# Optimization experiments

Hardware: AMD Instinct MI355X
Metric: run time of the kernel (lower is better)

## Reference

```python
import jax, jax.numpy as jnp
import numpy as np

DIM = 1024        # model dim
HEADS = 1         # num_heads (fc1 in_features==1 forces this)
HDIM = DIM // HEADS
INNER = 16        # dim_inner
B, L = 2, 4096
ROPE_BASE = 32.0


def _apply_rope(x, pos, base):
    # x: [b, l, h, d]; standard rotate-half RoPE
    d = x.shape[-1]
    inv_freq = base ** (-jnp.arange(0, d, 2, dtype=jnp.float32) / d)   # [d/2]
    ang = pos[:, None].astype(jnp.float32) * inv_freq                  # [l, d/2]
    emb = jnp.concatenate([ang, ang], axis=-1)                         # [l, d]
    cos = jnp.cos(emb)[None, :, None, :].astype(x.dtype)
    sin = jnp.sin(emb)[None, :, None, :].astype(x.dtype)
    x1, x2 = x[..., : d // 2], x[..., d // 2:]
    rot = jnp.concatenate([-x2, x1], axis=-1)
    return x * cos + rot * sin


def setup_inputs() -> dict:
    key = jax.random.key(0)
    ks = jax.random.split(key, 7)
    hidden_states = jax.random.normal(ks[0], (B, L, DIM), dtype=jnp.float32)
    Wq = jax.random.normal(ks[1], (DIM, DIM), dtype=jnp.float32) * 0.02
    Wk = jax.random.normal(ks[2], (DIM, DIM), dtype=jnp.float32) * 0.02
    fc1_w = jax.random.normal(ks[3], (INNER, 1), dtype=jnp.float32) * 0.1
    fc1_b = jax.random.normal(ks[4], (INNER,), dtype=jnp.float32) * 0.1
    fc2_w = jax.random.normal(ks[5], (DIM, INNER), dtype=jnp.float32) * 0.1
    fc2_b = jax.random.normal(ks[6], (DIM,), dtype=jnp.float32) * 0.1
    return {"hidden_states": hidden_states, "Wq": Wq, "Wk": Wk,
            "fc1_w": fc1_w, "fc1_b": fc1_b, "fc2_w": fc2_w, "fc2_b": fc2_b}


def reference(hidden_states, Wq, Wk, fc1_w, fc1_b, fc2_w, fc2_b):
    b, l, _ = hidden_states.shape
    # projections, cast to bf16 as in the torch module
    q = (hidden_states @ Wq.T).reshape(b, l, HEADS, HDIM).astype(jnp.bfloat16)
    k = (hidden_states @ Wk.T).reshape(b, l, HEADS, HDIM).astype(jnp.bfloat16)
    pos = jnp.arange(l)
    q = _apply_rope(q, pos, ROPE_BASE)
    k = _apply_rope(k, pos, ROPE_BASE)
    # causal exp(QK) with NO softmax normalization; accumulate in fp32
    scores = jnp.einsum('bqhd,bkhd->bhqk',
                        q.astype(jnp.float32), k.astype(jnp.float32)) / (HDIM ** 0.5)
    causal = jnp.tril(jnp.ones((l, l), dtype=bool))                    # [l, l]
    exp_qk = jnp.where(causal[None, None], jnp.exp(scores), 0.0)       # [b, h, l, l]
    o = jnp.swapaxes(exp_qk.sum(axis=-1), 1, 2)                        # [b, l, h]
    # small MLP: h(=1) -> INNER -> DIM
    o = jax.nn.relu(o @ fc1_w.T + fc1_b)
    return o @ fc2_w.T + fc2_b                                         # [b, l, DIM]
```

## Files before the change

kernel.cpp:

```cpp
#include <hip/hip_runtime.h>
#include <hip/hip_bf16.h>

typedef __bf16 bf16_t;
typedef __bf16 bf16x4 __attribute__((ext_vector_type(4)));
typedef __bf16 bf16x8 __attribute__((ext_vector_type(8)));
typedef float f32x4 __attribute__((ext_vector_type(4)));

#define B_   2
#define L_   4096
#define DIM_ 1024
#define M_   (B_ * L_)
#define MT_  (L_ / 128)
#define NTASK_ ((MT_ * (MT_ + 1)) / 2)

__device__ __forceinline__ void ld_g2l_16(const bf16_t* g, bf16_t* l) {
  __builtin_amdgcn_global_load_lds(
      (__attribute__((address_space(1))) void*)g,
      (__attribute__((address_space(3))) void*)l, 16, 0, 0);
}

__global__ void cvt_f32_bf16(const float* __restrict__ src,
                             bf16_t* __restrict__ dst, int n4) {
  int i = blockIdx.x * blockDim.x + threadIdx.x;
  if (i < n4) {
    float4 v = ((const float4*)src)[i];
    bf16x4 o = { (bf16_t)v.x, (bf16_t)v.y, (bf16_t)v.z, (bf16_t)v.w };
    ((bf16x4*)dst)[i] = o;
  }
}

__device__ __forceinline__ void mfma_bt_core(const bf16_t* __restrict__ A,
                                             const bf16_t* __restrict__ B,
                                             int K, bf16_t* As, bf16_t* Bs,
                                             f32x4 (&acc)[4][4]) {
  const int tid  = threadIdx.x;
  const int wave = tid >> 6, lane = tid & 63;
  const int quad = lane >> 4, l16 = lane & 15;
  const int wm = (wave >> 1) * 64, wn = (wave & 1) * 64;
  const int srow = lane >> 2;
  const int scol = (lane & 3) * 8;

  for (int kk = 0; kk < K; kk += 32) {
    __syncthreads();
#pragma unroll
    for (int c = 0; c < 2; ++c) {
      int seg = c * 4 + wave;
      int row = seg * 16 + srow;
      ld_g2l_16(A + (size_t)row * K + kk + scol, As + seg * 512);
      ld_g2l_16(B + (size_t)row * K + kk + scol, Bs + seg * 512);
    }
    __syncthreads();

    bf16x8 af[4], bfr[4];
#pragma unroll
    for (int i = 0; i < 4; ++i) {
      af[i]  = *(const bf16x8*)(As + (wm + i * 16 + l16) * 32 + quad * 8);
      bfr[i] = *(const bf16x8*)(Bs + (wn + i * 16 + l16) * 32 + quad * 8);
    }
#pragma unroll
    for (int i = 0; i < 4; ++i)
#pragma unroll
      for (int j = 0; j < 4; ++j)
        acc[i][j] = __builtin_amdgcn_mfma_f32_16x16x32_bf16(af[i], bfr[j],
                                                            acc[i][j], 0, 0, 0);
  }
}

__global__ __launch_bounds__(256)
void proj_gemm(const bf16_t* __restrict__ A, const bf16_t* __restrict__ Wqb,
               const bf16_t* __restrict__ Wkb, bf16_t* __restrict__ Cq,
               bf16_t* __restrict__ Ck) {
  const int K = DIM_, N = DIM_;
  const bf16_t* Bm = (blockIdx.z == 0) ? Wqb : Wkb;
  bf16_t* Cm = (blockIdx.z == 0) ? Cq : Ck;
  __shared__ __attribute__((aligned(16))) bf16_t As[128 * 32];
  __shared__ __attribute__((aligned(16))) bf16_t Bs[128 * 32];
  const int tid = threadIdx.x;
  const int wave = tid >> 6, lane = tid & 63;
  const int quad = lane >> 4, l16 = lane & 15;
  const int wm = (wave >> 1) * 64, wn = (wave & 1) * 64;
  const int m0 = blockIdx.y * 128, n0 = blockIdx.x * 128;

  f32x4 acc[4][4] = {};
  mfma_bt_core(A + (size_t)m0 * K, Bm + (size_t)n0 * K, K, As, Bs, acc);

#pragma unroll
  for (int i = 0; i < 4; ++i)
#pragma unroll
    for (int j = 0; j < 4; ++j)
#pragma unroll
      for (int r = 0; r < 4; ++r) {
        int m = m0 + wm + i * 16 + quad * 4 + r;
        int n = n0 + wn + j * 16 + l16;
        Cm[(size_t)m * N + n] = (bf16_t)acc[i][j][r];
      }
}

__global__ void rope_kernel(bf16_t* __restrict__ x) {
  int row = blockIdx.x * 2 + (threadIdx.x >> 7);
  int j0  = (threadIdx.x & 127) * 4;
  int pos = row & (L_ - 1);
  bf16_t* p = x + (size_t)row * DIM_;
  bf16x4 v1 = *(const bf16x4*)(p + j0);
  bf16x4 v2 = *(const bf16x4*)(p + j0 + 512);
  bf16x4 o1, o2;
#pragma unroll
  for (int u = 0; u < 4; ++u) {
    int j = j0 + u;
    float ang = (float)pos * exp2f((float)j * (-5.0f / 512.0f));
    float c = cosf(ang), s = sinf(ang);
    float cb = (float)(bf16_t)c, sb = (float)(bf16_t)s;
    float x1 = (float)v1[u], x2 = (float)v2[u];
    o1[u] = (bf16_t)(x1 * cb - x2 * sb);
    o2[u] = (bf16_t)(x2 * cb + x1 * sb);
  }
  *(bf16x4*)(p + j0) = o1;
  *(bf16x4*)(p + j0 + 512) = o2;
}

__global__ void zero_f32(float* p, int n) {
  int i = blockIdx.x * blockDim.x + threadIdx.x;
  if (i < n) p[i] = 0.0f;
}

__global__ __launch_bounds__(256)
void attn_rowsum(const bf16_t* __restrict__ Q, const bf16_t* __restrict__ Kc,
                 float* __restrict__ o) {
  int t = blockIdx.x;
  int b = t / NTASK_;
  t -= b * NTASK_;
  int mt = (int)((sqrtf(8.0f * (float)t + 1.0f) - 1.0f) * 0.5f);
  while ((mt + 1) * (mt + 2) / 2 <= t) ++mt;
  while (mt * (mt + 1) / 2 > t) --mt;
  int nt = t - mt * (mt + 1) / 2;

  __shared__ __attribute__((aligned(16))) bf16_t As[128 * 32];
  __shared__ __attribute__((aligned(16))) bf16_t Bs[128 * 32];
  const int tid = threadIdx.x;
  const int wave = tid >> 6, lane = tid & 63;
  const int quad = lane >> 4, l16 = lane & 15;
  const int wm = (wave >> 1) * 64, wn = (wave & 1) * 64;

  const bf16_t* A  = Q  + (size_t)b * L_ * DIM_ + (size_t)mt * 128 * DIM_;
  const bf16_t* Bp = Kc + (size_t)b * L_ * DIM_ + (size_t)nt * 128 * DIM_;

  f32x4 acc[4][4] = {};
  mfma_bt_core(A, Bp, DIM_, As, Bs, acc);

  const bool diag = (mt == nt);
#pragma unroll
  for (int i = 0; i < 4; ++i) {
#pragma unroll
    for (int r = 0; r < 4; ++r) {
      int mrow = wm + i * 16 + quad * 4 + r;
      float sum = 0.0f;
#pragma unroll
      for (int j = 0; j < 4; ++j) {
        int ncol = wn + j * 16 + l16;
        float e = __expf(acc[i][j][r] * 0.03125f);
        if (!diag || ncol <= mrow) sum += e;
      }
      sum += __shfl_xor(sum, 1);
      sum += __shfl_xor(sum, 2);
      sum += __shfl_xor(sum, 4);
      sum += __shfl_xor(sum, 8);
      if (l16 == 0)
        atomicAdd(&o[b * L_ + mt * 128 + mrow], sum);
    }
  }
}

__global__ __launch_bounds__(256)
void mlp_out_kernel(const float* __restrict__ o, const float* __restrict__ fc1_w,
                    const float* __restrict__ fc1_b, const float* __restrict__ fc2_w,
                    const float* __restrict__ fc2_b, float* __restrict__ out) {
  const int R = 16;
  int row0 = blockIdx.x * R;
  int tid = threadIdx.x;
  __shared__ float h[R][16];
  {
    int rl = tid >> 4, i = tid & 15;
    float s = o[row0 + rl];
    h[rl][i] = fmaxf(fc1_w[i] * s + fc1_b[i], 0.0f);
  }
  __syncthreads();
  int d = tid * 4;
  float w[4][16];
#pragma unroll
  for (int c = 0; c < 4; ++c)
#pragma unroll
    for (int i = 0; i < 16; ++i) w[c][i] = fc2_w[(d + c) * 16 + i];
  float4 bb = *(const float4*)(fc2_b + d);
  for (int rl = 0; rl < R; ++rl) {
    float4 v = bb;
#pragma unroll
    for (int i = 0; i < 16; ++i) {
      float hv = h[rl][i];
      v.x += w[0][i] * hv; v.y += w[1][i] * hv;
      v.z += w[2][i] * hv; v.w += w[3][i] * hv;
    }
    *(float4*)(out + (size_t)(row0 + rl) * DIM_ + d) = v;
  }
}

extern "C" void kernel_launch(void* const* d_in, const int* in_sizes, int n_in,
                              void* d_out, int out_size, void* d_ws, size_t ws_size,
                              hipStream_t stream) {
  const float* hs    = (const float*)d_in[0];
  const float* Wq    = (const float*)d_in[1];
  const float* Wk    = (const float*)d_in[2];
  const float* fc1_w = (const float*)d_in[3];
  const float* fc1_b = (const float*)d_in[4];
  const float* fc2_w = (const float*)d_in[5];
  const float* fc2_b = (const float*)d_in[6];
  float* out = (float*)d_out;

  char* ws = (char*)d_ws;
  bf16_t* hs_bf = (bf16_t*)ws; ws += (size_t)M_ * DIM_ * 2;
  bf16_t* wq_bf = (bf16_t*)ws; ws += (size_t)DIM_ * DIM_ * 2;
  bf16_t* wk_bf = (bf16_t*)ws; ws += (size_t)DIM_ * DIM_ * 2;
  bf16_t* q_bf  = (bf16_t*)ws; ws += (size_t)M_ * DIM_ * 2;
  bf16_t* k_bf  = (bf16_t*)ws; ws += (size_t)M_ * DIM_ * 2;
  float*  o     = (float*)ws;

  cvt_f32_bf16<<<M_ * DIM_ / 4 / 256, 256, 0, stream>>>(hs, hs_bf, M_ * DIM_ / 4);
  cvt_f32_bf16<<<DIM_ * DIM_ / 4 / 256, 256, 0, stream>>>(Wq, wq_bf, DIM_ * DIM_ / 4);
  cvt_f32_bf16<<<DIM_ * DIM_ / 4 / 256, 256, 0, stream>>>(Wk, wk_bf, DIM_ * DIM_ / 4);

  dim3 gg(DIM_ / 128, M_ / 128, 2);
  proj_gemm<<<gg, 256, 0, stream>>>(hs_bf, wq_bf, wk_bf, q_bf, k_bf);

  rope_kernel<<<M_ / 2, 256, 0, stream>>>(q_bf);
  rope_kernel<<<M_ / 2, 256, 0, stream>>>(k_bf);

  zero_f32<<<M_ / 256, 256, 0, stream>>>(o, M_);
  attn_rowsum<<<B_ * NTASK_, 256, 0, stream>>>(q_bf, k_bf, o);

  mlp_out_kernel<<<M_ / 16, 256, 0, stream>>>(o, fc1_w, fc1_b, fc2_w, fc2_b, out);
}
```

Measured before the change: 255.5 us.

## Enlarge GEMM tiles to 256x128 and merge small launches

Both the projection GEMM and the causal QK row-sum kernel move from 128x128 to 256x128 output tiles, with each wave owning 64 full rows and all 8 column fragments. This lets each K fragment feed more MFMAs and cuts redundant global/LDS traffic. The triangular task mapping is redone for 256-row Q tiles against 128-column K tiles, and the causal mask now compares global row and column indices. The three conversion kernels become one, the two RoPE launches become one 2-D grid, and the zero kernel becomes a memset, reducing launch count. Larger accumulators (128 floats per thread) raise register pressure, and fewer blocks may lower occupancy.

```diff
diff --git a/kernel.cpp b/kernel.cpp
--- a/kernel.cpp
+++ b/kernel.cpp
@@ -10,8 +10,7 @@
 #define L_   4096
 #define DIM_ 1024
 #define M_   (B_ * L_)
-#define MT_  (L_ / 128)
-#define NTASK_ ((MT_ * (MT_ + 1)) / 2)
+#define NTASK2_ 272
 
 __device__ __forceinline__ void ld_g2l_16(const bf16_t* g, bf16_t* l) {
   __builtin_amdgcn_global_load_lds(
@@ -19,84 +18,92 @@
       (__attribute__((address_space(3))) void*)l, 16, 0, 0);
 }
 
-__global__ void cvt_f32_bf16(const float* __restrict__ src,
-                             bf16_t* __restrict__ dst, int n4) {
+__global__ void cvt_all(const float* __restrict__ hs, const float* __restrict__ wq,
+                        const float* __restrict__ wk, bf16_t* __restrict__ hs_b,
+                        bf16_t* __restrict__ wq_b, bf16_t* __restrict__ wk_b) {
+  const int N_HS = M_ * DIM_ / 4, N_W = DIM_ * DIM_ / 4;
   int i = blockIdx.x * blockDim.x + threadIdx.x;
-  if (i < n4) {
-    float4 v = ((const float4*)src)[i];
-    bf16x4 o = { (bf16_t)v.x, (bf16_t)v.y, (bf16_t)v.z, (bf16_t)v.w };
-    ((bf16x4*)dst)[i] = o;
-  }
-}
-
-__device__ __forceinline__ void mfma_bt_core(const bf16_t* __restrict__ A,
+  const float* s; bf16_t* d; int idx;
+  if (i < N_HS)            { s = hs; d = hs_b; idx = i; }
+  else if (i < N_HS + N_W) { s = wq; d = wq_b; idx = i - N_HS; }
+  else                     { s = wk; d = wk_b; idx = i - N_HS - N_W; }
+  float4 v = ((const float4*)s)[idx];
+  bf16x4 o = { (bf16_t)v.x, (bf16_t)v.y, (bf16_t)v.z, (bf16_t)v.w };
+  ((bf16x4*)d)[idx] = o;
+}
+
+__device__ __forceinline__ void core_256x128(const bf16_t* __restrict__ A,
                                              const bf16_t* __restrict__ B,
                                              int K, bf16_t* As, bf16_t* Bs,
-                                             f32x4 (&acc)[4][4]) {
+                                             f32x4 (&acc)[4][8]) {
   const int tid  = threadIdx.x;
   const int wave = tid >> 6, lane = tid & 63;
   const int quad = lane >> 4, l16 = lane & 15;
-  const int wm = (wave >> 1) * 64, wn = (wave & 1) * 64;
   const int srow = lane >> 2;
   const int scol = (lane & 3) * 8;
 
   for (int kk = 0; kk < K; kk += 32) {
     __syncthreads();
 #pragma unroll
-    for (int c = 0; c < 2; ++c) {
+    for (int c = 0; c < 6; ++c) {
       int seg = c * 4 + wave;
-      int row = seg * 16 + srow;
-      ld_g2l_16(A + (size_t)row * K + kk + scol, As + seg * 512);
-      ld_g2l_16(B + (size_t)row * K + kk + scol, Bs + seg * 512);
+      if (seg < 16) {
+        int row = seg * 16 + srow;
+        ld_g2l_16(A + (size_t)row * K + kk + scol, As + seg * 512);
+      } else {
+        int row = (seg - 16) * 16 + srow;
+        ld_g2l_16(B + (size_t)row * K + kk + scol, Bs + (seg - 16) * 512);
+      }
     }
     __syncthreads();
 
-    bf16x8 af[4], bfr[4];
-#pragma unroll
-    for (int i = 0; i < 4; ++i) {
-      af[i]  = *(const bf16x8*)(As + (wm + i * 16 + l16) * 32 + quad * 8);
-      bfr[i] = *(const bf16x8*)(Bs + (wn + i * 16 + l16) * 32 + quad * 8);
-    }
+    bf16x8 af[4], bfr[8];
 #pragma unroll
     for (int i = 0; i < 4; ++i)
-#pragma unroll
-      for (int j = 0; j < 4; ++j)
+      af[i] = *(const bf16x8*)(As + (wave * 64 + i * 16 + l16) * 32 + quad * 8);
+#pragma unroll
+    for (int j = 0; j < 8; ++j)
+      bfr[j] = *(const bf16x8*)(Bs + (j * 16 + l16) * 32 + quad * 8);
+#pragma unroll
+    for (int i = 0; i < 4; ++i)
+#pragma unroll
+      for (int j = 0; j < 8; ++j)
         acc[i][j] = __builtin_amdgcn_mfma_f32_16x16x32_bf16(af[i], bfr[j],
                                                             acc[i][j], 0, 0, 0);
   }
 }
 
-__global__ __launch_bounds__(256)
+__global__ __launch_bounds__(256, 2)
 void proj_gemm(const bf16_t* __restrict__ A, const bf16_t* __restrict__ Wqb,
                const bf16_t* __restrict__ Wkb, bf16_t* __restrict__ Cq,
                bf16_t* __restrict__ Ck) {
   const int K = DIM_, N = DIM_;
   const bf16_t* Bm = (blockIdx.z == 0) ? Wqb : Wkb;
   bf16_t* Cm = (blockIdx.z == 0) ? Cq : Ck;
-  __shared__ __attribute__((aligned(16))) bf16_t As[128 * 32];
+  __shared__ __attribute__((aligned(16))) bf16_t As[256 * 32];
   __shared__ __attribute__((aligned(16))) bf16_t Bs[128 * 32];
   const int tid = threadIdx.x;
   const int wave = tid >> 6, lane = tid & 63;
   const int quad = lane >> 4, l16 = lane & 15;
-  const int wm = (wave >> 1) * 64, wn = (wave & 1) * 64;
-  const int m0 = blockIdx.y * 128, n0 = blockIdx.x * 128;
-
-  f32x4 acc[4][4] = {};
-  mfma_bt_core(A + (size_t)m0 * K, Bm + (size_t)n0 * K, K, As, Bs, acc);
+  const int m0 = blockIdx.y * 256, n0 = blockIdx.x * 128;
+
+  f32x4 acc[4][8] = {};
+  core_256x128(A + (size_t)m0 * K, Bm + (size_t)n0 * K, K, As, Bs, acc);
 
 #pragma unroll
   for (int i = 0; i < 4; ++i)
 #pragma unroll
-    for (int j = 0; j < 4; ++j)
+    for (int j = 0; j < 8; ++j)
 #pragma unroll
       for (int r = 0; r < 4; ++r) {
-        int m = m0 + wm + i * 16 + quad * 4 + r;
-        int n = n0 + wn + j * 16 + l16;
+        int m = m0 + wave * 64 + i * 16 + quad * 4 + r;
+        int n = n0 + j * 16 + l16;
         Cm[(size_t)m * N + n] = (bf16_t)acc[i][j][r];
       }
 }
 
-__global__ void rope_kernel(bf16_t* __restrict__ x) {
+__global__ void rope_kernel(bf16_t* __restrict__ q, bf16_t* __restrict__ k) {
+  bf16_t* x = blockIdx.y ? k : q;
   int row = blockIdx.x * 2 + (threadIdx.x >> 7);
   int j0  = (threadIdx.x & 127) * 4;
   int pos = row & (L_ - 1);
@@ -118,54 +125,48 @@
   *(bf16x4*)(p + j0 + 512) = o2;
 }
 
-__global__ void zero_f32(float* p, int n) {
-  int i = blockIdx.x * blockDim.x + threadIdx.x;
-  if (i < n) p[i] = 0.0f;
-}
-
-__global__ __launch_bounds__(256)
+__global__ __launch_bounds__(256, 2)
 void attn_rowsum(const bf16_t* __restrict__ Q, const bf16_t* __restrict__ Kc,
                  float* __restrict__ o) {
   int t = blockIdx.x;
-  int b = t / NTASK_;
-  t -= b * NTASK_;
-  int mt = (int)((sqrtf(8.0f * (float)t + 1.0f) - 1.0f) * 0.5f);
-  while ((mt + 1) * (mt + 2) / 2 <= t) ++mt;
-  while (mt * (mt + 1) / 2 > t) --mt;
-  int nt = t - mt * (mt + 1) / 2;
-
-  __shared__ __attribute__((aligned(16))) bf16_t As[128 * 32];
+  int b = t / NTASK2_;
+  t -= b * NTASK2_;
+  int mi = (int)((sqrtf(4.0f * (float)t + 1.0f) - 1.0f) * 0.5f);
+  while ((mi + 1) * (mi + 2) <= t) ++mi;
+  while (mi * (mi + 1) > t) --mi;
+  int nt = t - mi * (mi + 1);
+
+  __shared__ __attribute__((aligned(16))) bf16_t As[256 * 32];
   __shared__ __attribute__((aligned(16))) bf16_t Bs[128 * 32];
   const int tid = threadIdx.x;
   const int wave = tid >> 6, lane = tid & 63;
   const int quad = lane >> 4, l16 = lane & 15;
-  const int wm = (wave >> 1) * 64, wn = (wave & 1) * 64;
-
-  const bf16_t* A  = Q  + (size_t)b * L_ * DIM_ + (size_t)mt * 128 * DIM_;
+
+  const bf16_t* A  = Q  + (size_t)b * L_ * DIM_ + (size_t)mi * 256 * DIM_;
   const bf16_t* Bp = Kc + (size_t)b * L_ * DIM_ + (size_t)nt * 128 * DIM_;
 
-  f32x4 acc[4][4] = {};
-  mfma_bt_core(A, Bp, DIM_, As, Bs, acc);
-
-  const bool diag = (mt == nt);
+  f32x4 acc[4][8] = {};
+  core_256x128(A, Bp, DIM_, As, Bs, acc);
+
+  const bool masked = (nt >= 2 * mi);
 #pragma unroll
   for (int i = 0; i < 4; ++i) {
 #pragma unroll
     for (int r = 0; r < 4; ++r) {
-      int mrow = wm + i * 16 + quad * 4 + r;
+      int grow = mi * 256 + wave * 64 + i * 16 + quad * 4 + r;
       float sum = 0.0f;
 #pragma unroll
-      for (int j = 0; j < 4; ++j) {
-        int ncol = wn + j * 16 + l16;
+      for (int j = 0; j < 8; ++j) {
+        int gcol = nt * 128 + j * 16 + l16;
         float e = __expf(acc[i][j][r] * 0.03125f);
-        if (!diag || ncol <= mrow) sum += e;
+        if (!masked || gcol <= grow) sum += e;
       }
       sum += __shfl_xor(sum, 1);
       sum += __shfl_xor(sum, 2);
       sum += __shfl_xor(sum, 4);
       sum += __shfl_xor(sum, 8);
       if (l16 == 0)
-        atomicAdd(&o[b * L_ + mt * 128 + mrow], sum);
+        atomicAdd(&o[b * L_ + grow], sum);
     }
   }
 }
@@ -223,18 +224,17 @@
   bf16_t* k_bf  = (bf16_t*)ws; ws += (size_t)M_ * DIM_ * 2;
   float*  o     = (float*)ws;
 
-  cvt_f32_bf16<<<M_ * DIM_ / 4 / 256, 256, 0, stream>>>(hs, hs_bf, M_ * DIM_ / 4);
-  cvt_f32_bf16<<<DIM_ * DIM_ / 4 / 256, 256, 0, stream>>>(Wq, wq_bf, DIM_ * DIM_ / 4);
-  cvt_f32_bf16<<<DIM_ * DIM_ / 4 / 256, 256, 0, stream>>>(Wk, wk_bf, DIM_ * DIM_ / 4);
-
-  dim3 gg(DIM_ / 128, M_ / 128, 2);
+  const int n4 = (M_ * DIM_ + 2 * DIM_ * DIM_) / 4;
+  cvt_all<<<n4 / 256, 256, 0, stream>>>(hs, Wq, Wk, hs_bf, wq_bf, wk_bf);
+
+  dim3 gg(DIM_ / 128, M_ / 256, 2);
   proj_gemm<<<gg, 256, 0, stream>>>(hs_bf, wq_bf, wk_bf, q_bf, k_bf);
 
-  rope_kernel<<<M_ / 2, 256, 0, stream>>>(q_bf);
-  rope_kernel<<<M_ / 2, 256, 0, stream>>>(k_bf);
-
-  zero_f32<<<M_ / 256, 256, 0, stream>>>(o, M_);
-  attn_rowsum<<<B_ * NTASK_, 256, 0, stream>>>(q_bf, k_bf, o);
+  dim3 gr(M_ / 2, 2);
+  rope_kernel<<<gr, 256, 0, stream>>>(q_bf, k_bf);
+
+  hipMemsetAsync(o, 0, M_ * sizeof(float), stream);
+  attn_rowsum<<<B_ * NTASK2_, 256, 0, stream>>>(q_bf, k_bf, o);
 
   mlp_out_kernel<<<M_ / 16, 256, 0, stream>>>(o, fc1_w, fc1_b, fc2_w, fc2_b, out);
 }
```

After: 245.0 us. -4.1%, faster.
